# Kernel optimization log

Measured on AMD Instinct MI355X. Metric: run time of the kernel, lower is better.

The kernel has to match this reference:

```python
import jax, jax.numpy as jnp
from jax import lax
import numpy as np

VOCAB = 2048
EMB = 256
LAT = 128
MAX_SENLEN = 8
SIZE_LAT = 3.0
BATCH = 32


def lm_softmax(tokens, E, Wi, Wh, b):
    """Embedding(mask_zero) -> LSTM(units=VOCAB) -> softmax. tokens: [B, L] int."""
    B, L = tokens.shape
    emb = E[tokens]                      # [B, L, EMB]
    mask = (tokens != 0)                 # PAD==0 is masked (Keras mask_zero)
    H = Wh.shape[0]

    def step(carry, xm):
        h, c = carry
        x, m = xm                        # x: [B, EMB], m: [B]
        gates = x @ Wi + h @ Wh + b      # [B, 4H], Keras gate order i,f,g,o
        i, f, g, o = jnp.split(gates, 4, axis=1)
        i = jax.nn.sigmoid(i)
        f = jax.nn.sigmoid(f)
        g = jnp.tanh(g)
        o = jax.nn.sigmoid(o)
        c_new = f * c + i * g
        h_new = o * jnp.tanh(c_new)
        m = m[:, None]
        h = jnp.where(m, h_new, h)       # masked steps carry state through
        c = jnp.where(m, c_new, c)
        return (h, c), None

    h0 = jnp.zeros((B, H), emb.dtype)
    (h, _), _ = lax.scan(step, (h0, h0), (jnp.swapaxes(emb, 0, 1), mask.T))
    return jax.nn.softmax(h, axis=-1)    # [B, VOCAB]


def setup_inputs() -> dict:
    key = jax.random.key(0)
    k1, k2, k3, k4 = jax.random.split(key, 4)
    input_tokens = jax.random.randint(k1, (BATCH, MAX_SENLEN), 0, VOCAB, dtype=jnp.int32)
    E = jax.random.normal(k2, (VOCAB, EMB), jnp.float32) * 0.02
    Wi = jax.random.normal(k3, (EMB, 4 * VOCAB), jnp.float32) * 0.02
    Wh = jax.random.normal(k4, (VOCAB, 4 * VOCAB), jnp.float32) * 0.02
    b = jnp.zeros((4 * VOCAB,), jnp.float32).at[VOCAB:2 * VOCAB].set(1.0)  # unit_forget_bias
    return {"input_tokens": input_tokens, "E": E, "Wi": Wi, "Wh": Wh, "b": b}


def reference(input_tokens, E, Wi, Wh, b):
    """Unrolled DAriEL_Encoder_Cell_2 RNN: returns z sequence [B, T, LAT]."""
    B, T = input_tokens.shape
    tokens = jnp.zeros((B, T + 1), jnp.int32)        # tokens state, col 0 = PAD
    # RNN zero initial state: bounds both zero at t=0 (cond keeps them since timeStep==0)
    low = jnp.zeros((B, LAT), jnp.float32)
    upp = jnp.zeros((B, LAT), jnp.float32)
    outs = []
    for t in range(T):
        # replace_column(tokens, input_token, timeStep+1)
        tokens = tokens.at[:, t + 1].set(input_tokens[:, t])
        if t > 0:  # tf.cond(mean(timeStep) > 0, initial bounds, state bounds)
            low = jnp.zeros((B, LAT), jnp.float32)
            upp = jnp.full((B, LAT), SIZE_LAT, jnp.float32)
        sm = lm_softmax(tokens[:, : t + 1], E, Wi, Wh, b)   # LM on prefix s_0toj
        s_j = tokens[:, t + 1]                               # current token
        c_inc = jnp.cumsum(sm, axis=1)
        c_exc = c_inc - sm
        cu = jnp.take_along_axis(c_inc, s_j[:, None], axis=1)  # [B,1]
        cl = jnp.take_along_axis(c_exc, s_j[:, None], axis=1)  # [B,1]
        rng = upp - low
        new_low = low + rng * cl
        upp = low + rng * cu
        low = new_low
        z = (low + upp) * 0.5            # mean over stacked bounds
        outs.append(z)
    return jnp.stack(outs, axis=1)       # [B, T, LAT]
```

## Files before the change

### kernel.cpp

```cpp
#include <hip/hip_runtime.h>

#define BATCH 32
#define TT 8
#define VOCAB 2048
#define EMB 256
#define NG 8192
#define LAT 128
#define KTOT 2304
#define NKT 72
#define NJT 128

#define WSCALE 4096.0f
#define ASCALE 16.0f
#define DQ (1.0f/65536.0f)

typedef float f32x4 __attribute__((ext_vector_type(4)));

#define EAC_OFF 0
#define FLG_OFF 256
#define ZP_OFF  4368
#define SP_OFF  33040
#define AFX_OFF 61712
#define AFH_OFF 76048
#define BP_OFF  108816

#define AT_LD(p)    __hip_atomic_load((p),  __ATOMIC_RELAXED, __HIP_MEMORY_SCOPE_AGENT)
#define AT_ST(p,v)  __hip_atomic_store((p), (v), __ATOMIC_RELAXED, __HIP_MEMORY_SCOPE_AGENT)

__device__ __forceinline__ float sigmoidf_(float x){ return 1.f/(1.f+__expf(-x)); }
__device__ __forceinline__ float tanhf_(float x){
  x = fminf(fmaxf(x, -10.f), 10.f);
  float e = __expf(2.f*x);
  return (e-1.f)/(e+1.f);
}
__device__ __forceinline__ unsigned char f2e4m3(float f){
  const unsigned int u = __float_as_uint(f);
  const unsigned int sign = (u >> 24) & 0x80u;
  const unsigned int au = u & 0x7FFFFFFFu;
  const unsigned int r = au + 0x0007FFFFu + ((au >> 20) & 1u);
  unsigned int code = (((r >> 23) - 120u) << 3) | ((r >> 20) & 7u);
  code = (code > 0x7Eu) ? 0x7Eu : code;
  const float a = __uint_as_float(au);
  const unsigned int sub = (unsigned int)rintf(a * 512.0f);
  code = (au < 0x3C800000u) ? sub : code;
  return (unsigned char)(sign | code);
}

__global__ __launch_bounds__(256) void k_pack(
    const int* __restrict__ tok, const float* __restrict__ E,
    const float* __restrict__ Wi, const float* __restrict__ Wh,
    unsigned long long* __restrict__ Bp,
    unsigned long long* __restrict__ AfX, unsigned long long* __restrict__ AfH1,
    int* __restrict__ flg, float* __restrict__ out){
  const int tid = threadIdx.x;
  const int nb = blockIdx.x;
  const int kt = blockIdx.y;
  __shared__ unsigned char lds[32][64];
  {
    const int kl = tid >> 3;
    const int n0 = (tid & 7) * 8;
    const int k  = kt*32 + kl;
    const float* W = (k < EMB) ? (Wi + (size_t)k*NG) : (Wh + (size_t)(k-EMB)*NG);
    const float4 f0 = *(const float4*)(W + nb*64 + n0);
    const float4 f1 = *(const float4*)(W + nb*64 + n0 + 4);
    unsigned long long pk = 0ull;
    pk |= (unsigned long long)f2e4m3(f0.x*WSCALE);
    pk |= (unsigned long long)f2e4m3(f0.y*WSCALE) << 8;
    pk |= (unsigned long long)f2e4m3(f0.z*WSCALE) << 16;
    pk |= (unsigned long long)f2e4m3(f0.w*WSCALE) << 24;
    pk |= (unsigned long long)f2e4m3(f1.x*WSCALE) << 32;
    pk |= (unsigned long long)f2e4m3(f1.y*WSCALE) << 40;
    pk |= (unsigned long long)f2e4m3(f1.z*WSCALE) << 48;
    pk |= (unsigned long long)f2e4m3(f1.w*WSCALE) << 56;
    *(unsigned long long*)&lds[kl][n0] = pk;
  }
  __syncthreads();
  {
    const int ntl = tid >> 6, lane = tid & 63;
    const int kgrp = lane >> 4, n16 = lane & 15;
    unsigned long long pk = 0ull;
    #pragma unroll
    for (int p=0;p<8;p++)
      pk |= ((unsigned long long)lds[kgrp*8 + p][ntl*16 + n16]) << (8*p);
    Bp[((size_t)(nb*4 + ntl)*NKT + kt)*64 + lane] = pk;
  }
  const int i = (kt*128 + nb)*256 + tid;
  if (i < 7*32*32){
    const int s   = i >> 10;
    const int rem = i & 1023;
    const int b   = rem >> 5;
    const int kgi = rem & 31;
    const int tk  = tok[b*TT + s];
    const float4 e0 = *(const float4*)(E + (size_t)tk*EMB + kgi*8);
    const float4 e1 = *(const float4*)(E + (size_t)tk*EMB + kgi*8 + 4);
    unsigned long long pk = 0ull;
    pk |= (unsigned long long)f2e4m3(e0.x*ASCALE);
    pk |= (unsigned long long)f2e4m3(e0.y*ASCALE) << 8;
    pk |= (unsigned long long)f2e4m3(e0.z*ASCALE) << 16;
    pk |= (unsigned long long)f2e4m3(e0.w*ASCALE) << 24;
    pk |= (unsigned long long)f2e4m3(e1.x*ASCALE) << 32;
    pk |= (unsigned long long)f2e4m3(e1.y*ASCALE) << 40;
    pk |= (unsigned long long)f2e4m3(e1.z*ASCALE) << 48;
    pk |= (unsigned long long)f2e4m3(e1.w*ASCALE) << 56;
    AfX[((size_t)((s*2 + (b>>4))*8 + (kgi>>2)))*64 + (kgi&3)*16 + (b&15)] = pk;
  }
  if (i < 8192) AfH1[i] = 0ull;
  if (i < BATCH*LAT)
    out[(size_t)((i>>7)*TT + 0)*LAT + (i&(LAT-1))] = 0.f;
  if (i < 4096) flg[i] = 0;
}

__global__ __launch_bounds__(512, 2) void k_fused(
    const int* __restrict__ tok, const float* __restrict__ bias,
    float* __restrict__ out, float* __restrict__ Zp, float* __restrict__ Sp,
    float* __restrict__ Eac, const unsigned long long* __restrict__ AfX,
    unsigned long long* __restrict__ AfH, const unsigned long long* __restrict__ Bp,
    int* __restrict__ flg){
  const int tid = threadIdx.x;
  const int bid = blockIdx.x;
  const int jt = bid;
  const int wid = tid >> 6, lane = tid & 63;
  const int g = wid & 3, mh = wid >> 2;
  const int quad = lane >> 4, col = lane & 15;

  __shared__ float gsh[2][4][16][16];
  __shared__ long hlds[2][64][64];
  __shared__ unsigned char hsh[512];
  __shared__ float zsh[2];

  const long* __restrict__ BpV = (const long*)Bp;
  const size_t bbase = (size_t)(g*NJT + jt)*NKT*64 + lane;
  long Breg[NKT];
  #pragma unroll
  for (int i=0;i<NKT;i++) Breg[i] = BpV[bbase + (size_t)i*64];
  #pragma unroll
  for (int i=0;i<NKT;i++) asm volatile("" : "+v"(Breg[i]));

  const int b = tid >> 4, jj = tid & 15;
  const int b16 = b & 15, mhb = b >> 4;
  const int j = jt*16 + jj;
  const float bi  = bias[j];
  const float bff = bias[j + VOCAB];
  const float bgg = bias[j + 2*VOCAB];
  const float boo = bias[j + 3*VOCAB];
  int tokr[TT];
  #pragma unroll
  for (int q2=0;q2<TT;q2++) tokr[q2] = tok[b*TT + q2];
  const int hoff = mhb*256 + ((jj>>3)&1)*128 + b16*8 + (jj&7);
  float hreg = 0.f, creg = 0.f;

  for (int t=1; t<TT; t++){
    const long* __restrict__ aX = (const long*)AfX + (size_t)((t-1)*2 + mh)*512 + lane;
    f32x4 acc = {0,0,0,0};
    #pragma unroll
    for (int kt=0; kt<8; kt++)
      acc = __builtin_amdgcn_mfma_f32_16x16x32_fp8_fp8(aX[(size_t)kt*64], Breg[kt], acc, 0,0,0);

    if (t >= 2){
      const int want = t-1;
      if (tid < 64){
        for (;;){
          int done = 1;
          #pragma unroll
          for (int q2=0;q2<2;q2++)
            done &= (AT_LD(&flg[(tid*2+q2)*16]) >= want) ? 1 : 0;
          if (done) break;
          __builtin_amdgcn_s_sleep(1);
        }
      }
      asm volatile("" ::: "memory");
    }
    __syncthreads();

    {
      unsigned long long* aH = AfH + (size_t)(t&1)*8192 + (size_t)mh*4096;
      long hl[16];
      #pragma unroll
      for (int i=0;i<16;i++)
        hl[i] = (long)AT_LD(&aH[(size_t)(g*16+i)*64 + lane]);
      #pragma unroll
      for (int i=0;i<16;i++) hlds[mh][g*16+i][lane] = hl[i];
    }
    __syncthreads();

    #pragma unroll
    for (int kt=8; kt<NKT; kt++)
      acc = __builtin_amdgcn_mfma_f32_16x16x32_fp8_fp8(hlds[mh][kt-8][lane], Breg[kt], acc, 0,0,0);
    #pragma unroll
    for (int r=0;r<4;r++) gsh[mh][g][quad*4 + r][col] = acc[r];
    __syncthreads();

    const float ip = gsh[mhb][0][b16][jj]*DQ + bi;
    const float fp = gsh[mhb][1][b16][jj]*DQ + bff;
    const float gg = gsh[mhb][2][b16][jj]*DQ + bgg;
    const float op = gsh[mhb][3][b16][jj]*DQ + boo;
    const float cn = sigmoidf_(fp)*creg + sigmoidf_(ip)*tanhf_(gg);
    const float hn = sigmoidf_(op)*tanhf_(cn);
    if (tokr[t-1] != 0){ hreg = hn; creg = cn; }
    hsh[hoff] = f2e4m3(ASCALE*hreg);
    const int sj = tokr[t];
    const float e = __expf(hreg);
    if (j == sj) AT_ST(&Eac[(t-1)*32 + b], e);
    float z = e, s = (j < sj) ? e : 0.f;
    #pragma unroll
    for (int m=1; m<16; m<<=1){ z += __shfl_xor(z, m); s += __shfl_xor(s, m); }
    if (jj == 0){
      AT_ST(&Zp[((size_t)(t-1)*32 + b)*128 + jt], z);
      AT_ST(&Sp[((size_t)(t-1)*32 + b)*128 + jt], s);
    }
    __syncthreads();

    if (tid < 64){
      const int pm = tid >> 5, w = tid & 31;
      unsigned long long* dst =
        (unsigned long long*)((unsigned char*)AfH + (size_t)((t&1)^1)*65536
                              + (size_t)(pm*64 + (jt>>1))*512 + (size_t)(jt&1)*256);
      AT_ST(&dst[w], ((const unsigned long long*)hsh)[pm*32 + w]);
    }
    asm volatile("s_waitcnt vmcnt(0)" ::: "memory");
    __syncthreads();
    if (tid == 0) AT_ST(&flg[bid*16], t);

    if (t >= 2 && bid < BATCH){
      const int s = t-2;
      if (tid < 64){
        float zl = AT_LD(&Zp[((size_t)s*32+bid)*128 + tid])
                 + AT_LD(&Zp[((size_t)s*32+bid)*128 + tid + 64]);
        float sl = AT_LD(&Sp[((size_t)s*32+bid)*128 + tid])
                 + AT_LD(&Sp[((size_t)s*32+bid)*128 + tid + 64]);
        #pragma unroll
        for (int m=1; m<64; m<<=1){ zl += __shfl_xor(zl, m); sl += __shfl_xor(sl, m); }
        if (tid == 0){ zsh[0] = zl; zsh[1] = sl; }
      }
      __syncthreads();
      if (tid < LAT){
        const float Ej = AT_LD(&Eac[s*32 + bid]);
        out[((size_t)bid*TT + (t-1))*LAT + tid] = (3.f*zsh[1] + 1.5f*Ej)/zsh[0];
      }
    }
  }

  if (bid < BATCH){
    if (tid < 64){
      for (;;){
        int done = 1;
        #pragma unroll
        for (int q2=0;q2<2;q2++)
          done &= (AT_LD(&flg[(tid*2+q2)*16]) >= TT-1) ? 1 : 0;
        if (done) break;
        __builtin_amdgcn_s_sleep(1);
      }
    }
    asm volatile("" ::: "memory");
    __syncthreads();
    const int s = TT-2;
    if (tid < 64){
      float zl = AT_LD(&Zp[((size_t)s*32+bid)*128 + tid])
               + AT_LD(&Zp[((size_t)s*32+bid)*128 + tid + 64]);
      float sl = AT_LD(&Sp[((size_t)s*32+bid)*128 + tid])
               + AT_LD(&Sp[((size_t)s*32+bid)*128 + tid + 64]);
      #pragma unroll
      for (int m=1; m<64; m<<=1){ zl += __shfl_xor(zl, m); sl += __shfl_xor(sl, m); }
      if (tid == 0){ zsh[0] = zl; zsh[1] = sl; }
    }
    __syncthreads();
    if (tid < LAT){
      const float Ej = AT_LD(&Eac[s*32 + bid]);
      out[((size_t)bid*TT + (TT-1))*LAT + tid] = (3.f*zsh[1] + 1.5f*Ej)/zsh[0];
    }
  }
}

extern "C" void kernel_launch(void* const* d_in, const int* in_sizes, int n_in,
                              void* d_out, int out_size, void* d_ws, size_t ws_size,
                              hipStream_t stream){
  const int*   tok  = (const int*)d_in[0];
  const float* E    = (const float*)d_in[1];
  const float* Wi   = (const float*)d_in[2];
  const float* Wh   = (const float*)d_in[3];
  const float* bias = (const float*)d_in[4];
  float* out = (float*)d_out;
  float* ws  = (float*)d_ws;
  float* Eac = ws + EAC_OFF;
  int*   flg = (int*)(ws + FLG_OFF);
  float* Zp  = ws + ZP_OFF;
  float* Sp  = ws + SP_OFF;
  unsigned long long* AfX = (unsigned long long*)(ws + AFX_OFF);
  unsigned long long* AfH = (unsigned long long*)(ws + AFH_OFF);
  unsigned long long* Bp  = (unsigned long long*)(ws + BP_OFF);

  k_pack<<<dim3(128, NKT), 256, 0, stream>>>(tok, E, Wi, Wh, Bp, AfX, AfH + 8192,
                                             flg, out);
  k_fused<<<128, 512, 0, stream>>>(tok, bias, out, Zp, Sp, Eac, AfX, AfH, Bp, flg);
}
```

Baseline: 148.3 us.

## Halve fused block to 256 threads and stream weights from memory each step

```diff
diff --git a/kernel.cpp b/kernel.cpp
--- a/kernel.cpp
+++ b/kernel.cpp
@@ -110,7 +110,7 @@
   if (i < 4096) flg[i] = 0;
 }
 
-__global__ __launch_bounds__(512, 2) void k_fused(
+__global__ __launch_bounds__(256, 1) void k_fused(
     const int* __restrict__ tok, const float* __restrict__ bias,
     float* __restrict__ out, float* __restrict__ Zp, float* __restrict__ Sp,
     float* __restrict__ Eac, const unsigned long long* __restrict__ AfX,
@@ -119,8 +119,7 @@
   const int tid = threadIdx.x;
   const int bid = blockIdx.x;
   const int jt = bid;
-  const int wid = tid >> 6, lane = tid & 63;
-  const int g = wid & 3, mh = wid >> 2;
+  const int g = tid >> 6, lane = tid & 63;
   const int quad = lane >> 4, col = lane & 15;
 
   __shared__ float gsh[2][4][16][16];
@@ -130,31 +129,25 @@
 
   const long* __restrict__ BpV = (const long*)Bp;
   const size_t bbase = (size_t)(g*NJT + jt)*NKT*64 + lane;
-  long Breg[NKT];
-  #pragma unroll
-  for (int i=0;i<NKT;i++) Breg[i] = BpV[bbase + (size_t)i*64];
-  #pragma unroll
-  for (int i=0;i<NKT;i++) asm volatile("" : "+v"(Breg[i]));
-
-  const int b = tid >> 4, jj = tid & 15;
-  const int b16 = b & 15, mhb = b >> 4;
+
+  const int b16 = tid >> 4, jj = tid & 15;
   const int j = jt*16 + jj;
   const float bi  = bias[j];
   const float bff = bias[j + VOCAB];
   const float bgg = bias[j + 2*VOCAB];
   const float boo = bias[j + 3*VOCAB];
-  int tokr[TT];
-  #pragma unroll
-  for (int q2=0;q2<TT;q2++) tokr[q2] = tok[b*TT + q2];
-  const int hoff = mhb*256 + ((jj>>3)&1)*128 + b16*8 + (jj&7);
-  float hreg = 0.f, creg = 0.f;
+  const int hoff = ((jj>>3)&1)*128 + b16*8 + (jj&7);
+  float hreg0 = 0.f, creg0 = 0.f, hreg1 = 0.f, creg1 = 0.f;
 
   for (int t=1; t<TT; t++){
-    const long* __restrict__ aX = (const long*)AfX + (size_t)((t-1)*2 + mh)*512 + lane;
-    f32x4 acc = {0,0,0,0};
+    const long* __restrict__ aX = (const long*)AfX + (size_t)((t-1)*2)*512 + lane;
+    f32x4 acc0 = {0,0,0,0}, acc1 = {0,0,0,0};
     #pragma unroll
-    for (int kt=0; kt<8; kt++)
-      acc = __builtin_amdgcn_mfma_f32_16x16x32_fp8_fp8(aX[(size_t)kt*64], Breg[kt], acc, 0,0,0);
+    for (int kt=0; kt<8; kt++){
+      const long bv = BpV[bbase + (size_t)kt*64];
+      acc0 = __builtin_amdgcn_mfma_f32_16x16x32_fp8_fp8(aX[(size_t)kt*64], bv, acc0, 0,0,0);
+      acc1 = __builtin_amdgcn_mfma_f32_16x16x32_fp8_fp8(aX[(size_t)(512 + kt*64)], bv, acc1, 0,0,0);
+    }
 
     if (t >= 2){
       const int want = t-1;
@@ -173,40 +166,75 @@
     __syncthreads();
 
     {
-      unsigned long long* aH = AfH + (size_t)(t&1)*8192 + (size_t)mh*4096;
-      long hl[16];
-      #pragma unroll
-      for (int i=0;i<16;i++)
-        hl[i] = (long)AT_LD(&aH[(size_t)(g*16+i)*64 + lane]);
-      #pragma unroll
-      for (int i=0;i<16;i++) hlds[mh][g*16+i][lane] = hl[i];
+      unsigned long long* aH = AfH + (size_t)(t&1)*8192;
+      long hl0[16], hl1[16];
+      #pragma unroll
+      for (int i=0;i<16;i++){
+        hl0[i] = (long)AT_LD(&aH[(size_t)(g*16+i)*64 + lane]);
+        hl1[i] = (long)AT_LD(&aH[(size_t)(4096 + (g*16+i)*64) + lane]);
+      }
+      #pragma unroll
+      for (int i=0;i<16;i++){
+        hlds[0][g*16+i][lane] = hl0[i];
+        hlds[1][g*16+i][lane] = hl1[i];
+      }
     }
     __syncthreads();
 
     #pragma unroll
-    for (int kt=8; kt<NKT; kt++)
-      acc = __builtin_amdgcn_mfma_f32_16x16x32_fp8_fp8(hlds[mh][kt-8][lane], Breg[kt], acc, 0,0,0);
+    for (int kt=8; kt<NKT; kt++){
+      const long bv = BpV[bbase + (size_t)kt*64];
+      acc0 = __builtin_amdgcn_mfma_f32_16x16x32_fp8_fp8(hlds[0][kt-8][lane], bv, acc0, 0,0,0);
+      acc1 = __builtin_amdgcn_mfma_f32_16x16x32_fp8_fp8(hlds[1][kt-8][lane], bv, acc1, 0,0,0);
+    }
     #pragma unroll
-    for (int r=0;r<4;r++) gsh[mh][g][quad*4 + r][col] = acc[r];
-    __syncthreads();
-
-    const float ip = gsh[mhb][0][b16][jj]*DQ + bi;
-    const float fp = gsh[mhb][1][b16][jj]*DQ + bff;
-    const float gg = gsh[mhb][2][b16][jj]*DQ + bgg;
-    const float op = gsh[mhb][3][b16][jj]*DQ + boo;
-    const float cn = sigmoidf_(fp)*creg + sigmoidf_(ip)*tanhf_(gg);
-    const float hn = sigmoidf_(op)*tanhf_(cn);
-    if (tokr[t-1] != 0){ hreg = hn; creg = cn; }
-    hsh[hoff] = f2e4m3(ASCALE*hreg);
-    const int sj = tokr[t];
-    const float e = __expf(hreg);
-    if (j == sj) AT_ST(&Eac[(t-1)*32 + b], e);
-    float z = e, s = (j < sj) ? e : 0.f;
-    #pragma unroll
-    for (int m=1; m<16; m<<=1){ z += __shfl_xor(z, m); s += __shfl_xor(s, m); }
-    if (jj == 0){
-      AT_ST(&Zp[((size_t)(t-1)*32 + b)*128 + jt], z);
-      AT_ST(&Sp[((size_t)(t-1)*32 + b)*128 + jt], s);
+    for (int r=0;r<4;r++){
+      gsh[0][g][quad*4 + r][col] = acc0[r];
+      gsh[1][g][quad*4 + r][col] = acc1[r];
+    }
+    __syncthreads();
+
+    {
+      const int b0 = b16;
+      const float ip = gsh[0][0][b16][jj]*DQ + bi;
+      const float fp = gsh[0][1][b16][jj]*DQ + bff;
+      const float gg = gsh[0][2][b16][jj]*DQ + bgg;
+      const float op = gsh[0][3][b16][jj]*DQ + boo;
+      const float cn = sigmoidf_(fp)*creg0 + sigmoidf_(ip)*tanhf_(gg);
+      const float hn = sigmoidf_(op)*tanhf_(cn);
+      if (tok[b0*TT + (t-1)] != 0){ hreg0 = hn; creg0 = cn; }
+      hsh[hoff] = f2e4m3(ASCALE*hreg0);
+      const int sj = tok[b0*TT + t];
+      const float e = __expf(hreg0);
+      if (j == sj) AT_ST(&Eac[(t-1)*32 + b0], e);
+      float z = e, s = (j < sj) ? e : 0.f;
+      #pragma unroll
+      for (int m=1; m<16; m<<=1){ z += __shfl_xor(z, m); s += __shfl_xor(s, m); }
+      if (jj == 0){
+        AT_ST(&Zp[((size_t)(t-1)*32 + b0)*128 + jt], z);
+        AT_ST(&Sp[((size_t)(t-1)*32 + b0)*128 + jt], s);
+      }
+    }
+    {
+      const int b1 = 16 + b16;
+      const float ip = gsh[1][0][b16][jj]*DQ + bi;
+      const float fp = gsh[1][1][b16][jj]*DQ + bff;
+      const float gg = gsh[1][2][b16][jj]*DQ + bgg;
+      const float op = gsh[1][3][b16][jj]*DQ + boo;
+      const float cn = sigmoidf_(fp)*creg1 + sigmoidf_(ip)*tanhf_(gg);
+      const float hn = sigmoidf_(op)*tanhf_(cn);
+      if (tok[b1*TT + (t-1)] != 0){ hreg1 = hn; creg1 = cn; }
+      hsh[256 + hoff] = f2e4m3(ASCALE*hreg1);
+      const int sj = tok[b1*TT + t];
+      const float e = __expf(hreg1);
+      if (j == sj) AT_ST(&Eac[(t-1)*32 + b1], e);
+      float z = e, s = (j < sj) ? e : 0.f;
+      #pragma unroll
+      for (int m=1; m<16; m<<=1){ z += __shfl_xor(z, m); s += __shfl_xor(s, m); }
+      if (jj == 0){
+        AT_ST(&Zp[((size_t)(t-1)*32 + b1)*128 + jt], z);
+        AT_ST(&Sp[((size_t)(t-1)*32 + b1)*128 + jt], s);
+      }
     }
     __syncthreads();
 
@@ -291,5 +319,5 @@
 
   k_pack<<<dim3(128, NKT), 256, 0, stream>>>(tok, E, Wi, Wh, Bp, AfX, AfH + 8192,
                                              flg, out);
-  k_fused<<<128, 512, 0, stream>>>(tok, bias, out, Zp, Sp, Eac, AfX, AfH, Bp, flg);
-}
+  k_fused<<<128, 256, 0, stream>>>(tok, bias, out, Zp, Sp, Eac, AfX, AfH, Bp, flg);
+}
```

After: 157.8 us. 6.4% more time.
